# Kernel tuning notes

Measured on AMD Instinct MI355X. Metric: run time of the kernel, lower is better.

Reference implementation:

```python
import jax, jax.numpy as jnp
import numpy as np
import math

B, N = 1, 512
C_S, C_Z, C_H, H = 384, 128, 16, 12
P_Q, P_V, NBINS = 4, 8, 64
OUT_DIM = H * (C_H + P_V * 4 + C_Z)


def setup_inputs() -> dict:
    key = jax.random.key(0)
    ks = jax.random.split(key, 16)
    def rn(k, shape, scale=1.0):
        return jax.random.normal(k, shape, dtype=jnp.float32) * scale
    rotations, _ = jnp.linalg.qr(rn(ks[3], (B, N, 3, 3)))  # orthogonal frames
    w = 0.02
    return {
        "s": rn(ks[0], (B, N, C_S)),
        "z": rn(ks[1], (B, N, N, C_Z)),
        "translations": rn(ks[2], (B, N, 3), 10.0),  # spread over ~0-32 A bins
        "rotations": rotations,
        "Wq": rn(ks[4], (C_S, H * C_H), w), "bq": jnp.zeros((H * C_H,), jnp.float32),
        "Wk": rn(ks[5], (C_S, H * C_H), w), "bk": jnp.zeros((H * C_H,), jnp.float32),
        "Wv": rn(ks[6], (C_S, H * C_H), w), "bv": jnp.zeros((H * C_H,), jnp.float32),
        "Wqp": rn(ks[7], (C_S, H * P_Q * 3), w), "bqp": jnp.zeros((H * P_Q * 3,), jnp.float32),
        "Wkp": rn(ks[8], (C_S, H * P_Q * 3), w), "bkp": jnp.zeros((H * P_Q * 3,), jnp.float32),
        "Wvp": rn(ks[9], (C_S, H * P_V * 3), w), "bvp": jnp.zeros((H * P_V * 3,), jnp.float32),
        "Wb": rn(ks[10], (C_Z, H), w), "bb": jnp.zeros((H,), jnp.float32),
        "emb": rn(ks[11], (NBINS, H), w),
        "scale_logits": jnp.zeros((3, H), jnp.float32),
        "head_weights": jnp.ones((H,), jnp.float32),
        "Wout": rn(ks[12], (OUT_DIM, C_S), w), "bout": jnp.zeros((C_S,), jnp.float32),
    }


def reference(s, z, translations, rotations, Wq, bq, Wk, bk, Wv, bv, Wqp, bqp, Wkp, bkp, Wvp, bvp, Wb, bb, emb, scale_logits, head_weights, Wout, bout):
    b, n, _ = s.shape
    t = translations
    q = (s @ Wq + bq).reshape(b, n, H, C_H)
    k = (s @ Wk + bk).reshape(b, n, H, C_H)
    v = (s @ Wv + bv).reshape(b, n, H, C_H)
    q_pts = (s @ Wqp + bqp).reshape(b, n, H, P_Q, 3)
    k_pts = (s @ Wkp + bkp).reshape(b, n, H, P_Q, 3)
    v_pts = (s @ Wvp + bvp).reshape(b, n, H, P_V, 3)
    # local -> global frame
    q_g = jnp.einsum('bnij,bnhpj->bnhpi', rotations, q_pts) + t[:, :, None, None, :]
    k_g = jnp.einsum('bnij,bnhpj->bnhpi', rotations, k_pts) + t[:, :, None, None, :]
    v_g = jnp.einsum('bnij,bnhpj->bnhpi', rotations, v_pts) + t[:, :, None, None, :]
    scalar_logits = jnp.einsum('bnhc,bmhc->bnmh', q, k) / math.sqrt(C_H)  # [b,n,m,h]
    point_dist = jnp.sum((q_g[:, :, None] - k_g[:, None]) ** 2, axis=-1)  # [b,n,m,h,p]
    point_logits = -0.5 * jnp.sum(point_dist, axis=-1) * head_weights[None, None, None, :]
    pair_bias = z @ Wb + bb  # [b,n,m,h]
    pair_dist = jnp.linalg.norm(t[:, :, None, :] - t[:, None, :, :], axis=-1)  # [b,n,m]
    edges = jnp.linspace(0.0, 32.0, NBINS + 1)
    bins = jnp.clip(jnp.searchsorted(edges, pair_dist, side='left') - 1, 0, NBINS - 1)
    dist_bias = emb[bins]  # [b,n,m,h]
    scales = jnp.stack([
        (pair_dist <= 5.0).astype(s.dtype),
        ((pair_dist > 5.0) & (pair_dist <= 15.0)).astype(s.dtype),
        jnp.ones_like(pair_dist),
    ], axis=-1)  # [b,n,m,3]
    per_head = jax.nn.softmax(scale_logits, axis=0)  # [3,h]
    multiscale = jnp.einsum('bnms,sh->bnmh', scales, per_head)
    logits = scalar_logits + point_logits + pair_bias + dist_bias + multiscale
    attn = jax.nn.softmax(logits.astype(jnp.float32), axis=2).astype(s.dtype)  # over m
    out_scalar = jnp.einsum('bnmh,bmhc->bnhc', attn, v)
    out_pts_g = jnp.einsum('bnmh,bmhpi->bnhpi', attn, v_g)
    # global -> local frame (R^T applied)
    out_pts_l = jnp.einsum('bnji,bnhpj->bnhpi', rotations, out_pts_g - t[:, :, None, None, :])
    out_norms = jnp.linalg.norm(out_pts_l, axis=-1)  # [b,n,h,p]
    pair_feat = jnp.einsum('bnmh,bnmc->bnhc', attn, z)
    feats = jnp.concatenate([
        out_scalar,
        out_pts_l.reshape(b, n, H, P_V * 3),
        out_norms,
        pair_feat,
    ], axis=-1).reshape(b, n, -1)  # [b,n,OUT_DIM]
    return feats @ Wout + bout
```

## Files before the change

### kernel.cpp

```cpp
#include <hip/hip_runtime.h>

#define NTOK 512
#define CS 384
#define CZ 128
#define CH 16
#define HN 12
#define PQ 4
#define PV 8
#define FEAT_DIM 2112
#define HSEG 176

__global__ __launch_bounds__(256) void k_proj(
    const float* __restrict__ s,
    const float* __restrict__ Wq,  const float* __restrict__ bq,
    const float* __restrict__ Wk,  const float* __restrict__ bk,
    const float* __restrict__ Wv,  const float* __restrict__ bv,
    const float* __restrict__ Wqp, const float* __restrict__ bqp,
    const float* __restrict__ Wkp, const float* __restrict__ bkp,
    const float* __restrict__ Wvp, const float* __restrict__ bvp,
    float* __restrict__ qs, float* __restrict__ ksT, float* __restrict__ vs,
    float* __restrict__ raw_g)
{
    __shared__ float s_l[16 * CS];
    __shared__ float Ws[16][64];
    const int t  = threadIdx.x;
    const int n0 = blockIdx.x * 16;

    const float4* sg  = (const float4*)(s + (size_t)n0 * CS);
    float4*       sl4 = (float4*)s_l;
#pragma unroll
    for (int j = 0; j < 6; ++j) sl4[j * 256 + t] = sg[j * 256 + t];

    const int col = blockIdx.y * 64 + (t & 63);
    const int tq  = t >> 6;
    const float* bv_;
    int lc;
    if (col < 192)      { bv_ = bq;  lc = col;       }
    else if (col < 384) { bv_ = bk;  lc = col - 192; }
    else if (col < 576) { bv_ = bv;  lc = col - 384; }
    else if (col < 720) { bv_ = bqp; lc = col - 576; }
    else if (col < 864) { bv_ = bkp; lc = col - 720; }
    else                { bv_ = bvp; lc = col - 864; }

    const int kk_s = t >> 4, cq = t & 15;
    const int gcol = blockIdx.y * 64 + cq * 4;
    const float* Wsrc; int lcs, ncs;
    if (gcol < 192)      { Wsrc = Wq;  lcs = gcol;       ncs = 192; }
    else if (gcol < 384) { Wsrc = Wk;  lcs = gcol - 192; ncs = 192; }
    else if (gcol < 576) { Wsrc = Wv;  lcs = gcol - 384; ncs = 192; }
    else if (gcol < 720) { Wsrc = Wqp; lcs = gcol - 576; ncs = 144; }
    else if (gcol < 864) { Wsrc = Wkp; lcs = gcol - 720; ncs = 144; }
    else                 { Wsrc = Wvp; lcs = gcol - 864; ncs = 288; }

    float a0, a1, a2, a3;
    a0 = a1 = a2 = a3 = bv_[lc];
    __syncthreads();

    for (int ks = 0; ks < CS; ks += 16) {
        float4 w4 = *(const float4*)&Wsrc[(size_t)(ks + kk_s) * ncs + lcs];
        __syncthreads();
        *(float4*)&Ws[kk_s][cq * 4] = w4;
        __syncthreads();
        const float* srow = s_l + tq * 4 * CS + ks;
#pragma unroll
        for (int kk = 0; kk < 16; ++kk) {
            float w = Ws[kk][t & 63];
            a0 += srow[kk] * w;
            a1 += srow[CS + kk] * w;
            a2 += srow[2 * CS + kk] * w;
            a3 += srow[3 * CS + kk] * w;
        }
    }

    const int n = n0 + tq * 4;
    if (col < 192) {
        qs[(size_t)(n + 0) * 192 + lc] = a0;
        qs[(size_t)(n + 1) * 192 + lc] = a1;
        qs[(size_t)(n + 2) * 192 + lc] = a2;
        qs[(size_t)(n + 3) * 192 + lc] = a3;
    } else if (col < 384) {
        float* p = ksT + (size_t)lc * NTOK + n;
        p[0] = a0; p[1] = a1; p[2] = a2; p[3] = a3;
    } else if (col < 576) {
        vs[(size_t)(n + 0) * 192 + lc] = a0;
        vs[(size_t)(n + 1) * 192 + lc] = a1;
        vs[(size_t)(n + 2) * 192 + lc] = a2;
        vs[(size_t)(n + 3) * 192 + lc] = a3;
    } else {
        const int pc = col - 576;
        raw_g[(size_t)(n + 0) * 576 + pc] = a0;
        raw_g[(size_t)(n + 1) * 576 + pc] = a1;
        raw_g[(size_t)(n + 2) * 576 + pc] = a2;
        raw_g[(size_t)(n + 3) * 576 + pc] = a3;
    }
}

__global__ __launch_bounds__(256) void k_frame(
    const float* __restrict__ raw_g,
    const float* __restrict__ trans,
    const float* __restrict__ rot,
    float* __restrict__ qg, float* __restrict__ kgT, float* __restrict__ vg,
    float* __restrict__ transT)
{
    const int e = blockIdx.x * 256 + threadIdx.x;
    if (e < 512 * 576) {
        const int n = e / 576, loc = e % 576;
        const int i = loc % 3, base = loc - i;
        const float* rp = raw_g + (size_t)n * 576 + base;
        float x0 = rp[0], x1 = rp[1], x2 = rp[2];
        const float* R = rot + (size_t)n * 9 + i * 3;
        float v = trans[(size_t)n * 3 + i] + R[0] * x0 + R[1] * x1 + R[2] * x2;
        if (loc < 144)      qg[(size_t)n * 144 + loc] = v;
        else if (loc < 288) kgT[(size_t)(loc - 144) * NTOK + n] = v;
        else                vg[(size_t)n * 288 + loc - 288] = v;
    } else {
        const int idx = e - 512 * 576;
        if (idx < 3 * NTOK) {
            const int m = idx / 3, i = idx % 3;
            transT[(size_t)i * NTOK + m] = trans[(size_t)m * 3 + i];
        }
    }
}

__global__ __launch_bounds__(256) void k_bias(
    const float* __restrict__ z,
    const float* __restrict__ Wb,
    const float* __restrict__ bbv,
    float* __restrict__ bias)
{
    __shared__ float a_l[64 * 133];
    __shared__ float wb_l[CZ * HN];
    __shared__ float bb_l[HN];
    const int t = threadIdx.x;
    for (int i = t; i < CZ * HN; i += 256) wb_l[i] = Wb[i];
    if (t < HN) bb_l[t] = bbv[t];

    const float4* zg = (const float4*)(z + (size_t)blockIdx.x * 64 * CZ);
#pragma unroll
    for (int j = 0; j < 8; ++j) {
        const int f4i = j * 256 + t;
        const int row = f4i >> 5, c4 = f4i & 31;
        float4 v = zg[f4i];
        float* dst = &a_l[row * 133 + c4 * 4];
        dst[0] = v.x; dst[1] = v.y; dst[2] = v.z; dst[3] = v.w;
    }
    __syncthreads();

    const int row = t & 63;
    const int hg  = t >> 6;
    float acc0 = 0.f, acc1 = 0.f, acc2 = 0.f;
    const float* ar = &a_l[row * 133];
    const float* wr = wb_l + hg * 3;
#pragma unroll 8
    for (int c = 0; c < CZ; ++c) {
        float zc = ar[c];
        const float* w = wr + c * HN;
        acc0 += zc * w[0];
        acc1 += zc * w[1];
        acc2 += zc * w[2];
    }
    const int grow = blockIdx.x * 64 + row;
    const int n = grow >> 9, m = grow & 511;
    const int h = hg * 3;
    bias[((size_t)n * HN + h + 0) * NTOK + m] = acc0 + bb_l[h + 0];
    bias[((size_t)n * HN + h + 1) * NTOK + m] = acc1 + bb_l[h + 1];
    bias[((size_t)n * HN + h + 2) * NTOK + m] = acc2 + bb_l[h + 2];
}

__global__ __launch_bounds__(256) void k_attn(
    const float* __restrict__ qs, const float* __restrict__ ksT,
    const float* __restrict__ qg, const float* __restrict__ kgT,
    const float* __restrict__ trans, const float* __restrict__ transT,
    const float* __restrict__ emb,
    const float* __restrict__ slog,
    const float* __restrict__ hw,
    float* __restrict__ attn)
{
    const int n = blockIdx.x, h = blockIdx.y, t = threadIdx.x;
    __shared__ float ql[CH];
    __shared__ float qgl[12];
    __shared__ float tl[3];
    __shared__ float ph[3];
    __shared__ float red[8];
    __shared__ float emb_l[64];
    if (t < CH)       ql[t] = qs[(size_t)n * 192 + h * CH + t];
    else if (t < 28)  qgl[t - 16] = qg[(size_t)n * 144 + h * 12 + (t - 16)];
    else if (t < 31)  tl[t - 28] = trans[(size_t)n * 3 + (t - 28)];
    else if (t == 31) {
        float s0 = slog[0 * HN + h], s1 = slog[1 * HN + h], s2 = slog[2 * HN + h];
        float mx = fmaxf(s0, fmaxf(s1, s2));
        float e0 = expf(s0 - mx), e1 = expf(s1 - mx), e2 = expf(s2 - mx);
        float inv = 1.f / (e0 + e1 + e2);
        ph[0] = e0 * inv; ph[1] = e1 * inv; ph[2] = e2 * inv;
    } else if (t >= 64 && t < 128) {
        emb_l[t - 64] = emb[(size_t)(t - 64) * HN + h];
    }
    __syncthreads();

    const float hwv = hw[h];
    float* arow = attn + ((size_t)n * HN + h) * NTOK;
    const float* ksh = ksT + (size_t)h * CH * NTOK;
    const float* kgh = kgT + (size_t)h * 12 * NTOK;
    float lg[2];
#pragma unroll
    for (int r = 0; r < 2; ++r) {
        const int m = t + r * 256;
        float sc = 0.f;
#pragma unroll
        for (int c = 0; c < CH; ++c)
            sc += ql[c] * ksh[(size_t)c * NTOK + m];
        sc *= 0.25f;
        float sd = 0.f;
#pragma unroll
        for (int i = 0; i < 12; ++i) {
            float d = qgl[i] - kgh[(size_t)i * NTOK + m];
            sd += d * d;
        }
        float pl = -0.5f * sd * hwv;
        float dx = tl[0] - transT[m];
        float dy = tl[1] - transT[NTOK + m];
        float dz = tl[2] - transT[2 * NTOK + m];
        float dist = sqrtf(dx * dx + dy * dy + dz * dz);
        int bin = (int)ceilf(dist * 2.f) - 1;
        bin = min(63, max(0, bin));
        float db = emb_l[bin];
        float ms = ph[2] + (dist <= 5.f ? ph[0] : 0.f) + ((dist > 5.f && dist <= 15.f) ? ph[1] : 0.f);
        lg[r] = sc + pl + arow[m] + db + ms;
    }

    float mx = fmaxf(lg[0], lg[1]);
    for (int off = 32; off; off >>= 1) mx = fmaxf(mx, __shfl_down(mx, off));
    if ((t & 63) == 0) red[t >> 6] = mx;
    __syncthreads();
    if (t == 0) red[4] = fmaxf(fmaxf(red[0], red[1]), fmaxf(red[2], red[3]));
    __syncthreads();
    mx = red[4];
    float e0 = expf(lg[0] - mx), e1 = expf(lg[1] - mx);
    float sm = e0 + e1;
    for (int off = 32; off; off >>= 1) sm += __shfl_down(sm, off);
    if ((t & 63) == 0) red[t >> 6] = sm;
    __syncthreads();
    if (t == 0) red[5] = red[0] + red[1] + red[2] + red[3];
    __syncthreads();
    const float inv = 1.f / red[5];
    arow[t] = e0 * inv;
    arow[t + 256] = e1 * inv;
}

__global__ __launch_bounds__(256) void k_outmm(
    const float* __restrict__ attn,
    const float* __restrict__ vs, const float* __restrict__ vg,
    const float* __restrict__ trans,
    const float* __restrict__ rot,
    float* __restrict__ feats)
{
    __shared__ float As_t[64][33];
    __shared__ float Vs[64][40];
    __shared__ float out_l[32 * 40];
    __shared__ float Rl[32][9];
    __shared__ float tl[32][3];
    const int t   = threadIdx.x;
    const int gn0 = blockIdx.x * 32;
    const int h   = blockIdx.y;

    const int slab  = t >> 6;
    const int w     = t & 63;
    const int n0l   = (w >> 3) * 4;
    const int j0    = (w & 7) * 5;

    float acc[4][5];
#pragma unroll
    for (int i = 0; i < 4; ++i)
#pragma unroll
        for (int k = 0; k < 5; ++k) acc[i][k] = 0.f;

    for (int step = 0; step < 8; ++step) {
        const int mb = step * 64;
        __syncthreads();
#pragma unroll
        for (int jj = 0; jj < 2; ++jj) {
            const int f = t + jj * 256;
            const int n_loc = f >> 4, c4 = f & 15;
            float4 a = *(const float4*)&attn[(((size_t)(gn0 + n_loc)) * HN + h) * NTOK + mb + c4 * 4];
            As_t[c4 * 4 + 0][n_loc] = a.x;
            As_t[c4 * 4 + 1][n_loc] = a.y;
            As_t[c4 * 4 + 2][n_loc] = a.z;
            As_t[c4 * 4 + 3][n_loc] = a.w;
        }
#pragma unroll
        for (int jj = 0; jj < 10; ++jj) {
            const int f = t + jj * 256;
            const int m_loc = f / 40, jv = f % 40;
            float v;
            if (jv < 16) v = vs[(size_t)(mb + m_loc) * 192 + h * 16 + jv];
            else         v = vg[(size_t)(mb + m_loc) * 288 + h * 24 + (jv - 16)];
            Vs[m_loc][jv] = v;
        }
        __syncthreads();
#pragma unroll
        for (int mi = 0; mi < 16; ++mi) {
            const int m = slab * 16 + mi;
            float4 a = *(const float4*)&As_t[m][n0l];
            float vv[5];
#pragma unroll
            for (int k = 0; k < 5; ++k) vv[k] = Vs[m][j0 + k];
            const float av[4] = {a.x, a.y, a.z, a.w};
#pragma unroll
            for (int i = 0; i < 4; ++i)
#pragma unroll
                for (int k = 0; k < 5; ++k)
                    acc[i][k] += av[i] * vv[k];
        }
    }

    for (int s = 0; s < 4; ++s) {
        __syncthreads();
        if (slab == s) {
#pragma unroll
            for (int i = 0; i < 4; ++i)
#pragma unroll
                for (int k = 0; k < 5; ++k) {
                    float* p = &out_l[(n0l + i) * 40 + j0 + k];
                    if (s == 0) *p = acc[i][k];
                    else        *p += acc[i][k];
                }
        }
    }
    for (int i = t; i < 32 * 12; i += 256) {
        const int n_loc = i / 12, r = i % 12;
        if (r < 9) Rl[n_loc][r] = rot[(size_t)(gn0 + n_loc) * 9 + r];
        else       tl[n_loc][r - 9] = trans[(size_t)(gn0 + n_loc) * 3 + (r - 9)];
    }
    __syncthreads();

    for (int f = t; f < 32 * 48; f += 256) {
        const int n_loc = f / 48, j = f % 48;
        const float* sh = &out_l[n_loc * 40];
        float* fp = feats + (size_t)(gn0 + n_loc) * FEAT_DIM + h * HSEG;
        const float* R = Rl[n_loc];
        const float* tv = tl[n_loc];
        if (j < 16) {
            fp[j] = sh[j];
        } else if (j < 40) {
            const int jj = j - 16, p = jj / 3, i = jj % 3;
            float val = 0.f;
#pragma unroll
            for (int q = 0; q < 3; ++q) val += R[q * 3 + i] * (sh[16 + p * 3 + q] - tv[q]);
            fp[16 + jj] = val;
        } else {
            const int p = j - 40;
            float s2 = 0.f;
#pragma unroll
            for (int i = 0; i < 3; ++i) {
                float val = 0.f;
#pragma unroll
                for (int q = 0; q < 3; ++q) val += R[q * 3 + i] * (sh[16 + p * 3 + q] - tv[q]);
                s2 += val * val;
            }
            fp[40 + p] = sqrtf(s2);
        }
    }
}

__global__ __launch_bounds__(256) void k_pairfeat(
    const float* __restrict__ attn,
    const float* __restrict__ z,
    float* __restrict__ feats)
{
    __shared__ float a_l[HN * NTOK];
    __shared__ float out_l[HN * CZ];
    const int n = blockIdx.x, t = threadIdx.x;
    for (int i = t; i < HN * NTOK; i += 256) a_l[i] = attn[(size_t)n * HN * NTOK + i];
    __syncthreads();

    const int slab = t >> 6, lane = t & 63;
    const int c2 = lane * 2;
    float acc[HN][2];
#pragma unroll
    for (int h = 0; h < HN; ++h) { acc[h][0] = 0.f; acc[h][1] = 0.f; }

    const float* zp = z + (size_t)n * NTOK * CZ + (size_t)slab * 128 * CZ + c2;
    const float* ap = a_l + slab * 128;
#pragma unroll 4
    for (int m = 0; m < 128; ++m) {
        float2 zv = *(const float2*)(zp + (size_t)m * CZ);
#pragma unroll
        for (int h = 0; h < HN; ++h) {
            float a = ap[h * NTOK + m];
            acc[h][0] += a * zv.x;
            acc[h][1] += a * zv.y;
        }
    }
    for (int s = 0; s < 4; ++s) {
        __syncthreads();
        if (slab == s) {
#pragma unroll
            for (int h = 0; h < HN; ++h) {
                float* p = &out_l[h * CZ + c2];
                if (s == 0) { p[0] = acc[h][0]; p[1] = acc[h][1]; }
                else        { p[0] += acc[h][0]; p[1] += acc[h][1]; }
            }
        }
    }
    __syncthreads();
    for (int i = t; i < HN * CZ; i += 256) {
        const int h = i >> 7, c = i & 127;
        feats[(size_t)n * FEAT_DIM + h * HSEG + 48 + c] = out_l[i];
    }
}

#define KT 16
__global__ __launch_bounds__(256) void k_outproj(
    const float* __restrict__ feats,
    const float* __restrict__ Wout,
    const float* __restrict__ bout,
    float* __restrict__ out)
{
    __shared__ float As[KT][64];
    __shared__ float Bs[KT][64];
    const int t  = threadIdx.x;
    const int n0 = blockIdx.x * 64;
    const int j0 = blockIdx.y * 64;
    const int k0 = blockIdx.z * HSEG;

    const int arow = t >> 2, akq = (t & 3) * 4;
    const int bkk  = t >> 4, bjq = (t & 15) * 4;
    const int tr   = t >> 4, tc  = t & 15;

    float acc[4][4] = {{0.f}};
    for (int s = 0; s < 11; ++s) {
        const int ks = k0 + s * KT;
        float4 a4 = *(const float4*)&feats[(size_t)(n0 + arow) * FEAT_DIM + ks + akq];
        float4 b4 = *(const float4*)&Wout[(size_t)(ks + bkk) * 384 + j0 + bjq];
        __syncthreads();
        As[akq + 0][arow] = a4.x;
        As[akq + 1][arow] = a4.y;
        As[akq + 2][arow] = a4.z;
        As[akq + 3][arow] = a4.w;
        *(float4*)&Bs[bkk][bjq] = b4;
        __syncthreads();
#pragma unroll
        for (int kk = 0; kk < KT; ++kk) {
            float4 av = *(const float4*)&As[kk][tr * 4];
            float4 bv = *(const float4*)&Bs[kk][tc * 4];
            acc[0][0] += av.x * bv.x; acc[0][1] += av.x * bv.y;
            acc[0][2] += av.x * bv.z; acc[0][3] += av.x * bv.w;
            acc[1][0] += av.y * bv.x; acc[1][1] += av.y * bv.y;
            acc[1][2] += av.y * bv.z; acc[1][3] += av.y * bv.w;
            acc[2][0] += av.z * bv.x; acc[2][1] += av.z * bv.y;
            acc[2][2] += av.z * bv.z; acc[2][3] += av.z * bv.w;
            acc[3][0] += av.w * bv.x; acc[3][1] += av.w * bv.y;
            acc[3][2] += av.w * bv.z; acc[3][3] += av.w * bv.w;
        }
    }

    const bool addb = (blockIdx.z == 0);
#pragma unroll
    for (int i = 0; i < 4; ++i) {
        const int row = n0 + tr * 4 + i;
#pragma unroll
        for (int jj = 0; jj < 4; ++jj) {
            const int col = j0 + tc * 4 + jj;
            float v = acc[i][jj];
            if (addb) v += bout[col];
            atomicAdd(&out[(size_t)row * 384 + col], v);
        }
    }
}

extern "C" void kernel_launch(void* const* d_in, const int* in_sizes, int n_in,
                              void* d_out, int out_size, void* d_ws, size_t ws_size,
                              hipStream_t stream) {
    const float* s     = (const float*)d_in[0];
    const float* z     = (const float*)d_in[1];
    const float* trans = (const float*)d_in[2];
    const float* rot   = (const float*)d_in[3];
    const float* Wq    = (const float*)d_in[4];
    const float* bq    = (const float*)d_in[5];
    const float* Wk    = (const float*)d_in[6];
    const float* bk    = (const float*)d_in[7];
    const float* Wv    = (const float*)d_in[8];
    const float* bv    = (const float*)d_in[9];
    const float* Wqp   = (const float*)d_in[10];
    const float* bqp   = (const float*)d_in[11];
    const float* Wkp   = (const float*)d_in[12];
    const float* bkp   = (const float*)d_in[13];
    const float* Wvp   = (const float*)d_in[14];
    const float* bvp   = (const float*)d_in[15];
    const float* Wb    = (const float*)d_in[16];
    const float* bb    = (const float*)d_in[17];
    const float* emb   = (const float*)d_in[18];
    const float* slog  = (const float*)d_in[19];
    const float* hw    = (const float*)d_in[20];
    const float* Wout  = (const float*)d_in[21];
    const float* bout  = (const float*)d_in[22];

    float* W = (float*)d_ws;
    float* qs     = W;
    float* ksT    = qs + 98304;
    float* vs     = ksT + 98304;
    float* qg     = vs + 98304;
    float* kgT    = qg + 73728;
    float* vg     = kgT + 73728;
    float* transT = vg + 147456;
    float* bias   = transT + 1536;
    float* feats  = bias + 3145728;
    float* raw_g  = feats + 1081344;

    k_proj<<<dim3(32, 18), 256, 0, stream>>>(s, Wq, bq, Wk, bk, Wv, bv,
                                             Wqp, bqp, Wkp, bkp, Wvp, bvp,
                                             qs, ksT, vs, raw_g);
    k_frame<<<1158, 256, 0, stream>>>(raw_g, trans, rot, qg, kgT, vg, transT);
    k_bias<<<4096, 256, 0, stream>>>(z, Wb, bb, bias);
    k_attn<<<dim3(512, 12), 256, 0, stream>>>(qs, ksT, qg, kgT, trans, transT,
                                              emb, slog, hw, bias);
    k_outmm<<<dim3(16, 12), 256, 0, stream>>>(bias, vs, vg, trans, rot, feats);
    k_pairfeat<<<512, 256, 0, stream>>>(bias, z, feats);
    hipMemsetAsync(d_out, 0, (size_t)NTOK * 384 * sizeof(float), stream);
    k_outproj<<<dim3(8, 6, 12), 256, 0, stream>>>(feats, Wout, bout, (float*)d_out);
}
```

Measured before the change: 400.0 us.

## Fuse pair bias, attention softmax, and pair-feature reduction into one per-row kernel

```diff
diff --git a/kernel.cpp b/kernel.cpp
--- a/kernel.cpp
+++ b/kernel.cpp
@@ -122,129 +122,179 @@
     }
 }
 
-__global__ __launch_bounds__(256) void k_bias(
+__global__ __launch_bounds__(256) void k_mid(
     const float* __restrict__ z,
-    const float* __restrict__ Wb,
-    const float* __restrict__ bbv,
-    float* __restrict__ bias)
-{
-    __shared__ float a_l[64 * 133];
-    __shared__ float wb_l[CZ * HN];
-    __shared__ float bb_l[HN];
-    const int t = threadIdx.x;
-    for (int i = t; i < CZ * HN; i += 256) wb_l[i] = Wb[i];
-    if (t < HN) bb_l[t] = bbv[t];
-
-    const float4* zg = (const float4*)(z + (size_t)blockIdx.x * 64 * CZ);
-#pragma unroll
-    for (int j = 0; j < 8; ++j) {
-        const int f4i = j * 256 + t;
-        const int row = f4i >> 5, c4 = f4i & 31;
-        float4 v = zg[f4i];
-        float* dst = &a_l[row * 133 + c4 * 4];
-        dst[0] = v.x; dst[1] = v.y; dst[2] = v.z; dst[3] = v.w;
-    }
-    __syncthreads();
-
-    const int row = t & 63;
-    const int hg  = t >> 6;
-    float acc0 = 0.f, acc1 = 0.f, acc2 = 0.f;
-    const float* ar = &a_l[row * 133];
-    const float* wr = wb_l + hg * 3;
-#pragma unroll 8
-    for (int c = 0; c < CZ; ++c) {
-        float zc = ar[c];
-        const float* w = wr + c * HN;
-        acc0 += zc * w[0];
-        acc1 += zc * w[1];
-        acc2 += zc * w[2];
-    }
-    const int grow = blockIdx.x * 64 + row;
-    const int n = grow >> 9, m = grow & 511;
-    const int h = hg * 3;
-    bias[((size_t)n * HN + h + 0) * NTOK + m] = acc0 + bb_l[h + 0];
-    bias[((size_t)n * HN + h + 1) * NTOK + m] = acc1 + bb_l[h + 1];
-    bias[((size_t)n * HN + h + 2) * NTOK + m] = acc2 + bb_l[h + 2];
-}
-
-__global__ __launch_bounds__(256) void k_attn(
     const float* __restrict__ qs, const float* __restrict__ ksT,
     const float* __restrict__ qg, const float* __restrict__ kgT,
     const float* __restrict__ trans, const float* __restrict__ transT,
-    const float* __restrict__ emb,
-    const float* __restrict__ slog,
+    const float* __restrict__ Wb, const float* __restrict__ bbv,
+    const float* __restrict__ emb, const float* __restrict__ slog,
     const float* __restrict__ hw,
-    float* __restrict__ attn)
+    float* __restrict__ attn, float* __restrict__ feats)
 {
-    const int n = blockIdx.x, h = blockIdx.y, t = threadIdx.x;
-    __shared__ float ql[CH];
-    __shared__ float qgl[12];
+    __shared__ float lg[HN * NTOK];
+    __shared__ float zl[128 * 66];
+    __shared__ float wbl[CZ * HN];
+    __shared__ float embl[64 * HN];
+    __shared__ float ql[192];
+    __shared__ float qgl[144];
     __shared__ float tl[3];
-    __shared__ float ph[3];
-    __shared__ float red[8];
-    __shared__ float emb_l[64];
-    if (t < CH)       ql[t] = qs[(size_t)n * 192 + h * CH + t];
-    else if (t < 28)  qgl[t - 16] = qg[(size_t)n * 144 + h * 12 + (t - 16)];
-    else if (t < 31)  tl[t - 28] = trans[(size_t)n * 3 + (t - 28)];
-    else if (t == 31) {
-        float s0 = slog[0 * HN + h], s1 = slog[1 * HN + h], s2 = slog[2 * HN + h];
+    __shared__ float phl[36];
+    __shared__ float hwl[HN];
+
+    const int n = blockIdx.x, t = threadIdx.x;
+
+    for (int i = t; i < CZ * HN; i += 256) wbl[i] = Wb[i];
+    for (int i = t; i < 64 * HN; i += 256) embl[i] = emb[i];
+    if (t < 192) ql[t] = qs[(size_t)n * 192 + t];
+    if (t < 144) qgl[t] = qg[(size_t)n * 144 + t];
+    if (t < 3)   tl[t] = trans[(size_t)n * 3 + t];
+    if (t < HN)  hwl[t] = hw[t];
+    if (t >= 64 && t < 64 + HN) {
+        const int h = t - 64;
+        float s0 = slog[h], s1 = slog[HN + h], s2 = slog[2 * HN + h];
         float mx = fmaxf(s0, fmaxf(s1, s2));
         float e0 = expf(s0 - mx), e1 = expf(s1 - mx), e2 = expf(s2 - mx);
         float inv = 1.f / (e0 + e1 + e2);
-        ph[0] = e0 * inv; ph[1] = e1 * inv; ph[2] = e2 * inv;
-    } else if (t >= 64 && t < 128) {
-        emb_l[t - 64] = emb[(size_t)(t - 64) * HN + h];
+        phl[h] = e0 * inv; phl[12 + h] = e1 * inv; phl[24 + h] = e2 * inv;
+    }
+
+    const int ml = t & 63, hg = t >> 6, h0 = hg * 3;
+    const float bb0 = bbv[h0], bb1 = bbv[h0 + 1], bb2 = bbv[h0 + 2];
+
+    float4 pf[8];
+    {
+        const float4* zg = (const float4*)(z + (size_t)n * NTOK * CZ);
+#pragma unroll
+        for (int j = 0; j < 8; ++j) pf[j] = zg[j * 256 + t];
     }
     __syncthreads();
 
-    const float hwv = hw[h];
-    float* arow = attn + ((size_t)n * HN + h) * NTOK;
-    const float* ksh = ksT + (size_t)h * CH * NTOK;
-    const float* kgh = kgT + (size_t)h * 12 * NTOK;
-    float lg[2];
-#pragma unroll
-    for (int r = 0; r < 2; ++r) {
-        const int m = t + r * 256;
-        float sc = 0.f;
-#pragma unroll
-        for (int c = 0; c < CH; ++c)
-            sc += ql[c] * ksh[(size_t)c * NTOK + m];
-        sc *= 0.25f;
-        float sd = 0.f;
-#pragma unroll
-        for (int i = 0; i < 12; ++i) {
-            float d = qgl[i] - kgh[(size_t)i * NTOK + m];
-            sd += d * d;
-        }
-        float pl = -0.5f * sd * hwv;
-        float dx = tl[0] - transT[m];
-        float dy = tl[1] - transT[NTOK + m];
-        float dz = tl[2] - transT[2 * NTOK + m];
+    for (int mc = 0; mc < 8; ++mc) {
+#pragma unroll
+        for (int j = 0; j < 8; ++j) {
+            const int f = j * 256 + t;
+            const int mm = f >> 5, c4 = (f & 31) * 4;
+            float4 v = pf[j];
+            zl[(c4 + 0) * 66 + mm] = v.x;
+            zl[(c4 + 1) * 66 + mm] = v.y;
+            zl[(c4 + 2) * 66 + mm] = v.z;
+            zl[(c4 + 3) * 66 + mm] = v.w;
+        }
+        if (mc < 7) {
+            const float4* zg = (const float4*)(z + ((size_t)n * NTOK + (mc + 1) * 64) * CZ);
+#pragma unroll
+            for (int j = 0; j < 8; ++j) pf[j] = zg[j * 256 + t];
+        }
+        __syncthreads();
+
+        const int mg = mc * 64 + ml;
+        float b0 = bb0, b1 = bb1, b2 = bb2;
+        const float* zc = zl + ml;
+#pragma unroll 8
+        for (int c = 0; c < CZ; ++c) {
+            float zv = zc[c * 66];
+            const float* w = wbl + c * HN + h0;
+            b0 += zv * w[0];
+            b1 += zv * w[1];
+            b2 += zv * w[2];
+        }
+        float dx = tl[0] - transT[mg];
+        float dy = tl[1] - transT[NTOK + mg];
+        float dz = tl[2] - transT[2 * NTOK + mg];
         float dist = sqrtf(dx * dx + dy * dy + dz * dz);
-        int bin = (int)ceilf(dist * 2.f) - 1;
-        bin = min(63, max(0, bin));
-        float db = emb_l[bin];
-        float ms = ph[2] + (dist <= 5.f ? ph[0] : 0.f) + ((dist > 5.f && dist <= 15.f) ? ph[1] : 0.f);
-        lg[r] = sc + pl + arow[m] + db + ms;
-    }
-
-    float mx = fmaxf(lg[0], lg[1]);
-    for (int off = 32; off; off >>= 1) mx = fmaxf(mx, __shfl_down(mx, off));
-    if ((t & 63) == 0) red[t >> 6] = mx;
+        int bin = min(63, max(0, (int)ceilf(dist * 2.f) - 1));
+        const float in5  = (dist <= 5.f) ? 1.f : 0.f;
+        const float in15 = (dist > 5.f && dist <= 15.f) ? 1.f : 0.f;
+
+        float acc[3] = {b0, b1, b2};
+#pragma unroll
+        for (int k = 0; k < 3; ++k) {
+            const int h = h0 + k;
+            float sc = 0.f;
+            const float* kk = ksT + (size_t)h * CH * NTOK + mg;
+            const float* qq = ql + h * CH;
+#pragma unroll
+            for (int c = 0; c < CH; ++c) sc += qq[c] * kk[(size_t)c * NTOK];
+            float sd = 0.f;
+            const float* kg = kgT + (size_t)h * 12 * NTOK + mg;
+            const float* qp = qgl + h * 12;
+#pragma unroll
+            for (int i = 0; i < 12; ++i) {
+                float d = qp[i] - kg[(size_t)i * NTOK];
+                sd += d * d;
+            }
+            acc[k] += sc * 0.25f - 0.5f * sd * hwl[h]
+                    + embl[bin * HN + h]
+                    + phl[24 + h] + in5 * phl[h] + in15 * phl[12 + h];
+        }
+        lg[(h0 + 0) * NTOK + mg] = acc[0];
+        lg[(h0 + 1) * NTOK + mg] = acc[1];
+        lg[(h0 + 2) * NTOK + mg] = acc[2];
+        __syncthreads();
+    }
+
+    const int lane = t & 63;
+#pragma unroll
+    for (int hh = 0; hh < 3; ++hh) {
+        const int h = hg * 3 + hh;
+        float* row = lg + h * NTOK;
+        float v[8];
+        float mx = -1e30f;
+#pragma unroll
+        for (int i = 0; i < 8; ++i) { v[i] = row[lane + 64 * i]; mx = fmaxf(mx, v[i]); }
+#pragma unroll
+        for (int off = 32; off; off >>= 1) mx = fmaxf(mx, __shfl_xor(mx, off));
+        float sm = 0.f;
+#pragma unroll
+        for (int i = 0; i < 8; ++i) { v[i] = expf(v[i] - mx); sm += v[i]; }
+#pragma unroll
+        for (int off = 32; off; off >>= 1) sm += __shfl_xor(sm, off);
+        const float inv = 1.f / sm;
+        float* arow = attn + ((size_t)n * HN + h) * NTOK;
+#pragma unroll
+        for (int i = 0; i < 8; ++i) {
+            float a = v[i] * inv;
+            row[lane + 64 * i] = a;
+            arow[lane + 64 * i] = a;
+        }
+    }
     __syncthreads();
-    if (t == 0) red[4] = fmaxf(fmaxf(red[0], red[1]), fmaxf(red[2], red[3]));
+
+    const int slab = t >> 6;
+    const int c2 = (t & 63) * 2;
+    float pacc[HN][2];
+#pragma unroll
+    for (int h = 0; h < HN; ++h) { pacc[h][0] = 0.f; pacc[h][1] = 0.f; }
+    const float* zp = z + (size_t)n * NTOK * CZ + (size_t)slab * 128 * CZ + c2;
+    const float* ap = lg + slab * 128;
+#pragma unroll 4
+    for (int m = 0; m < 128; ++m) {
+        float2 zv = *(const float2*)(zp + (size_t)m * CZ);
+#pragma unroll
+        for (int h = 0; h < HN; ++h) {
+            float a = ap[h * NTOK + m];
+            pacc[h][0] += a * zv.x;
+            pacc[h][1] += a * zv.y;
+        }
+    }
+    float* out_l = zl;
+    for (int s = 0; s < 4; ++s) {
+        __syncthreads();
+        if (slab == s) {
+#pragma unroll
+            for (int h = 0; h < HN; ++h) {
+                float* p = &out_l[h * CZ + c2];
+                if (s == 0) { p[0] = pacc[h][0]; p[1] = pacc[h][1]; }
+                else        { p[0] += pacc[h][0]; p[1] += pacc[h][1]; }
+            }
+        }
+    }
     __syncthreads();
-    mx = red[4];
-    float e0 = expf(lg[0] - mx), e1 = expf(lg[1] - mx);
-    float sm = e0 + e1;
-    for (int off = 32; off; off >>= 1) sm += __shfl_down(sm, off);
-    if ((t & 63) == 0) red[t >> 6] = sm;
-    __syncthreads();
-    if (t == 0) red[5] = red[0] + red[1] + red[2] + red[3];
-    __syncthreads();
-    const float inv = 1.f / red[5];
-    arow[t] = e0 * inv;
-    arow[t + 256] = e1 * inv;
+    for (int i = t; i < HN * CZ; i += 256) {
+        const int h = i >> 7, c = i & 127;
+        feats[(size_t)n * FEAT_DIM + h * HSEG + 48 + c] = out_l[i];
+    }
 }
 
 __global__ __launch_bounds__(256) void k_outmm(
@@ -359,53 +409,6 @@
             }
             fp[40 + p] = sqrtf(s2);
         }
-    }
-}
-
-__global__ __launch_bounds__(256) void k_pairfeat(
-    const float* __restrict__ attn,
-    const float* __restrict__ z,
-    float* __restrict__ feats)
-{
-    __shared__ float a_l[HN * NTOK];
-    __shared__ float out_l[HN * CZ];
-    const int n = blockIdx.x, t = threadIdx.x;
-    for (int i = t; i < HN * NTOK; i += 256) a_l[i] = attn[(size_t)n * HN * NTOK + i];
-    __syncthreads();
-
-    const int slab = t >> 6, lane = t & 63;
-    const int c2 = lane * 2;
-    float acc[HN][2];
-#pragma unroll
-    for (int h = 0; h < HN; ++h) { acc[h][0] = 0.f; acc[h][1] = 0.f; }
-
-    const float* zp = z + (size_t)n * NTOK * CZ + (size_t)slab * 128 * CZ + c2;
-    const float* ap = a_l + slab * 128;
-#pragma unroll 4
-    for (int m = 0; m < 128; ++m) {
-        float2 zv = *(const float2*)(zp + (size_t)m * CZ);
-#pragma unroll
-        for (int h = 0; h < HN; ++h) {
-            float a = ap[h * NTOK + m];
-            acc[h][0] += a * zv.x;
-            acc[h][1] += a * zv.y;
-        }
-    }
-    for (int s = 0; s < 4; ++s) {
-        __syncthreads();
-        if (slab == s) {
-#pragma unroll
-            for (int h = 0; h < HN; ++h) {
-                float* p = &out_l[h * CZ + c2];
-                if (s == 0) { p[0] = acc[h][0]; p[1] = acc[h][1]; }
-                else        { p[0] += acc[h][0]; p[1] += acc[h][1]; }
-            }
-        }
-    }
-    __syncthreads();
-    for (int i = t; i < HN * CZ; i += 256) {
-        const int h = i >> 7, c = i & 127;
-        feats[(size_t)n * FEAT_DIM + h * HSEG + 48 + c] = out_l[i];
     }
 }
 
@@ -503,19 +506,17 @@
     float* kgT    = qg + 73728;
     float* vg     = kgT + 73728;
     float* transT = vg + 147456;
-    float* bias   = transT + 1536;
-    float* feats  = bias + 3145728;
+    float* attn   = transT + 1536;
+    float* feats  = attn + 3145728;
     float* raw_g  = feats + 1081344;
 
     k_proj<<<dim3(32, 18), 256, 0, stream>>>(s, Wq, bq, Wk, bk, Wv, bv,
                                              Wqp, bqp, Wkp, bkp, Wvp, bvp,
                                              qs, ksT, vs, raw_g);
     k_frame<<<1158, 256, 0, stream>>>(raw_g, trans, rot, qg, kgT, vg, transT);
-    k_bias<<<4096, 256, 0, stream>>>(z, Wb, bb, bias);
-    k_attn<<<dim3(512, 12), 256, 0, stream>>>(qs, ksT, qg, kgT, trans, transT,
-                                              emb, slog, hw, bias);
-    k_outmm<<<dim3(16, 12), 256, 0, stream>>>(bias, vs, vg, trans, rot, feats);
-    k_pairfeat<<<512, 256, 0, stream>>>(bias, z, feats);
+    k_mid<<<512, 256, 0, stream>>>(z, qs, ksT, qg, kgT, trans, transT,
+                                   Wb, bb, emb, slog, hw, attn, feats);
+    k_outmm<<<dim3(16, 12), 256, 0, stream>>>(attn, vs, vg, trans, rot, feats);
     hipMemsetAsync(d_out, 0, (size_t)NTOK * 384 * sizeof(float), stream);
     k_outproj<<<dim3(8, 6, 12), 256, 0, stream>>>(feats, Wout, bout, (float*)d_out);
 }
```

Result: no change. 398.9 us (-0.3%).
